# Kernel optimization log

Hardware: AMD Instinct MI355X
Metric: run time of the kernel (lower is better)

Reference implementation:

```python
import jax, jax.numpy as jnp
import numpy as np

N = 5000          # ngenes / nodes
IN_DIM = 1280
H = 128           # hid_dim
E = 160000        # edges (before self-loops)
ALPHA = 0.2       # LeakyReLU slope (both module leakyrelu and GATv2 negative_slope)

def _glorot(key, shape):
    fan_in, fan_out = shape[0], shape[-1]
    lim = jnp.sqrt(6.0 / (fan_in + fan_out))
    return jax.random.uniform(key, shape, jnp.float32, -lim, lim)

def setup_inputs() -> dict:
    key = jax.random.key(0)
    ks = jax.random.split(key, 12)
    x = jax.random.normal(ks[0], (N, IN_DIM), jnp.float32)
    edge_index = jax.random.randint(ks[1], (2, E), 0, N, jnp.int64)
    return {
        "x": x,
        "edge_index": edge_index,
        "W_in": _glorot(ks[2], (IN_DIM, H)),
        "b_in": jnp.zeros((H,), jnp.float32),
        "W_l": _glorot(ks[3], (H, H)),
        "b_l": jnp.zeros((H,), jnp.float32),
        "W_r": _glorot(ks[4], (H, H)),
        "b_r": jnp.zeros((H,), jnp.float32),
        "att": _glorot(ks[5], (H, 1))[:, 0],
        "gat_bias": jnp.zeros((H,), jnp.float32),
        "W1": _glorot(ks[6], (N * H, H)),
        "b1": jnp.zeros((H,), jnp.float32),
        "W2": _glorot(ks[7], (H, 1)),
        "b2": jnp.zeros((1,), jnp.float32),
    }

def _leaky(v):
    return jnp.where(v >= 0, v, ALPHA * v)

def _gatv2(x, edge_index, W_l, b_l, W_r, b_r, att, gat_bias):
    # add self loops (PyG default)
    loop = jnp.arange(N, dtype=edge_index.dtype)
    src = jnp.concatenate([edge_index[0], loop])  # j: source of message
    dst = jnp.concatenate([edge_index[1], loop])  # i: target / softmax segment
    xl = x @ W_l + b_l                             # [N, H] (messages)
    xr = x @ W_r + b_r                             # [N, H] (target side)
    e = _leaky(xl[src] + xr[dst])                  # [E+N, H]
    score = e @ att                                # [E+N]
    # segment softmax over incoming edges of each dst node
    m = jax.ops.segment_max(score, dst, num_segments=N)
    ex = jnp.exp(score - m[dst])
    s = jax.ops.segment_sum(ex, dst, num_segments=N)
    a = ex / s[dst]                                # [E+N]
    out = jax.ops.segment_sum(a[:, None] * xl[src], dst, num_segments=N)
    return out + gat_bias

def reference(x, edge_index, W_in, b_in, W_l, b_l, W_r, b_r, att, gat_bias, W1, b1, W2, b2):
    h = jax.nn.relu(x @ W_in + b_in)                               # [N, H]
    h = _leaky(_gatv2(h, edge_index, W_l, b_l, W_r, b_r, att, gat_bias))
    h = h.reshape(-1)                                              # [N*H]
    h = jax.nn.relu(h @ W1 + b1)                                   # [H]
    return h @ W2 + b2                                             # [1]
```

## Files before the change

### kernel.cpp

```cpp
#include <hip/hip_runtime.h>
#include <math.h>

#define N_NODES 5000
#define IN_DIM  1280
#define HID     128
#define ALPHA   0.2f

__device__ __forceinline__ float leaky(float v) { return v >= 0.f ? v : ALPHA * v; }

__global__ __launch_bounds__(256) void k_gemm_in(const float* __restrict__ x,
    const float* __restrict__ W, float* __restrict__ hp) {
  const int col  = threadIdx.x & 127;
  const int rg   = threadIdx.x >> 7;
  const int row0 = blockIdx.x * 16;
  const int kbase = blockIdx.y * 640;
  __shared__ float xs[16][128];
  float acc[8] = {0.f,0.f,0.f,0.f,0.f,0.f,0.f,0.f};
  for (int k0 = 0; k0 < 640; k0 += 128) {
#pragma unroll
    for (int t = 0; t < 8; ++t) {
      int idx = threadIdx.x + t * 256;
      int r = idx >> 7, c = idx & 127;
      int row = row0 + r;
      xs[r][c] = (row < N_NODES) ? x[(size_t)row * IN_DIM + kbase + k0 + c] : 0.f;
    }
    __syncthreads();
#pragma unroll 8
    for (int kq = 0; kq < 32; ++kq) {
      const int kk = kbase + k0 + kq * 4;
      const float w0 = W[(kk + 0) * HID + col];
      const float w1 = W[(kk + 1) * HID + col];
      const float w2 = W[(kk + 2) * HID + col];
      const float w3 = W[(kk + 3) * HID + col];
#pragma unroll
      for (int r = 0; r < 8; ++r) {
        const float4 xv = *reinterpret_cast<const float4*>(&xs[rg * 8 + r][kq * 4]);
        acc[r] = fmaf(xv.x, w0, acc[r]);
        acc[r] = fmaf(xv.y, w1, acc[r]);
        acc[r] = fmaf(xv.z, w2, acc[r]);
        acc[r] = fmaf(xv.w, w3, acc[r]);
      }
    }
    __syncthreads();
  }
  float* out = hp + (size_t)blockIdx.y * N_NODES * HID;
#pragma unroll
  for (int r = 0; r < 8; ++r) {
    int row = row0 + rg * 8 + r;
    if (row < N_NODES) out[(size_t)row * HID + col] = acc[r];
  }
}

__global__ __launch_bounds__(256) void k_gemm_lr(const float* __restrict__ hp,
    const float* __restrict__ bin,
    const float* __restrict__ Wl, const float* __restrict__ bl,
    const float* __restrict__ Wr, const float* __restrict__ br,
    float* __restrict__ xl, float* __restrict__ xr) {
  const int col  = threadIdx.x & 127;
  const int rg   = threadIdx.x >> 7;
  const int row0 = blockIdx.x * 8;
  __shared__ float hs[8][128];
  const float* hp0 = hp;
  const float* hp1 = hp + (size_t)N_NODES * HID;
#pragma unroll
  for (int t = 0; t < 4; ++t) {
    int idx = threadIdx.x + t * 256;
    int r = idx >> 7, c = idx & 127;
    size_t g = (size_t)(row0 + r) * HID + c;
    hs[r][c] = fmaxf(hp0[g] + hp1[g] + bin[c], 0.f);
  }
  __syncthreads();
  float accl[4] = {0.f,0.f,0.f,0.f};
  float accr[4] = {0.f,0.f,0.f,0.f};
#pragma unroll 4
  for (int kq = 0; kq < 32; ++kq) {
    float wl0 = Wl[(kq*4+0)*HID + col], wr0 = Wr[(kq*4+0)*HID + col];
    float wl1 = Wl[(kq*4+1)*HID + col], wr1 = Wr[(kq*4+1)*HID + col];
    float wl2 = Wl[(kq*4+2)*HID + col], wr2 = Wr[(kq*4+2)*HID + col];
    float wl3 = Wl[(kq*4+3)*HID + col], wr3 = Wr[(kq*4+3)*HID + col];
#pragma unroll
    for (int r = 0; r < 4; ++r) {
      const float4 xv = *reinterpret_cast<const float4*>(&hs[rg*4 + r][kq*4]);
      accl[r] = fmaf(xv.x, wl0, accl[r]); accr[r] = fmaf(xv.x, wr0, accr[r]);
      accl[r] = fmaf(xv.y, wl1, accl[r]); accr[r] = fmaf(xv.y, wr1, accr[r]);
      accl[r] = fmaf(xv.z, wl2, accl[r]); accr[r] = fmaf(xv.z, wr2, accr[r]);
      accl[r] = fmaf(xv.w, wl3, accl[r]); accr[r] = fmaf(xv.w, wr3, accr[r]);
    }
  }
  const float biasl = bl[col], biasr = br[col];
#pragma unroll
  for (int r = 0; r < 4; ++r) {
    int row = row0 + rg * 4 + r;
    xl[(size_t)row * HID + col] = accl[r] + biasl;
    xr[(size_t)row * HID + col] = accr[r] + biasr;
  }
}

__global__ __launch_bounds__(256) void k_hist(const int* __restrict__ ei, int E, int ET,
                                              unsigned* __restrict__ deg) {
  int e = blockIdx.x * blockDim.x + threadIdx.x;
  if (e >= ET) return;
  const int dst = (e < E) ? ei[E + e] : (e - E);
  atomicAdd(&deg[dst], 1u);
}

__global__ __launch_bounds__(256) void k_scan(const unsigned* __restrict__ deg,
    unsigned* __restrict__ off, unsigned* __restrict__ cursor) {
  __shared__ unsigned part[256];
  const int t = threadIdx.x;
  unsigned s = 0;
#pragma unroll
  for (int i = 0; i < 20; ++i) { int d = t * 20 + i; if (d < N_NODES) s += deg[d]; }
  part[t] = s;
  __syncthreads();
  for (int st = 1; st < 256; st <<= 1) {
    unsigned val = (t >= st) ? part[t - st] : 0u;
    __syncthreads();
    part[t] += val;
    __syncthreads();
  }
  unsigned run = (t == 0) ? 0u : part[t - 1];
  for (int i = 0; i < 20; ++i) {
    int d = t * 20 + i;
    if (d < N_NODES) { off[d] = run; cursor[d] = run; run += deg[d]; }
  }
}

__global__ __launch_bounds__(256) void k_fill(const int* __restrict__ ei, int E, int ET,
    unsigned* __restrict__ cursor, unsigned* __restrict__ csr) {
  int e = blockIdx.x * blockDim.x + threadIdx.x;
  if (e >= ET) return;
  const int src = (e < E) ? ei[e]     : (e - E);
  const int dst = (e < E) ? ei[E + e] : (e - E);
  unsigned pos = atomicAdd(&cursor[dst], 1u);
  csr[pos] = (unsigned)src;
}

__global__ __launch_bounds__(64) void k_agg(const float* __restrict__ xl,
    const float* __restrict__ xr, const float* __restrict__ att,
    const float* __restrict__ gb, const unsigned* __restrict__ off,
    const unsigned* __restrict__ deg, const unsigned* __restrict__ csr,
    float* __restrict__ v) {
  const int dst  = blockIdx.x;
  const int lane = threadIdx.x;
  const unsigned o  = off[dst];
  const unsigned dg = deg[dst];
  const float2 xr2 = *reinterpret_cast<const float2*>(&xr[(size_t)dst * HID + lane * 2]);
  const float2 at2 = *reinterpret_cast<const float2*>(&att[lane * 2]);
  float m = -INFINITY, s = 0.f;
  float2 acc = make_float2(0.f, 0.f);
  for (unsigned t = 0; t < dg; ++t) {
    const unsigned src = csr[o + t];
    const float2 xl2 = *reinterpret_cast<const float2*>(&xl[(size_t)src * HID + lane * 2]);
    float sa = leaky(xl2.x + xr2.x) * at2.x + leaky(xl2.y + xr2.y) * at2.y;
#pragma unroll
    for (int st = 1; st < 64; st <<= 1) sa += __shfl_xor(sa, st);
    if (sa > m) {
      const float sc = __expf(m - sa);
      s = s * sc + 1.f;
      acc.x = acc.x * sc + xl2.x;
      acc.y = acc.y * sc + xl2.y;
      m = sa;
    } else {
      const float ex = __expf(sa - m);
      s += ex;
      acc.x = fmaf(ex, xl2.x, acc.x);
      acc.y = fmaf(ex, xl2.y, acc.y);
    }
  }
  const float inv = 1.f / s;
  const float2 gb2 = *reinterpret_cast<const float2*>(&gb[lane * 2]);
  float2 r;
  r.x = leaky(fmaf(acc.x, inv, gb2.x));
  r.y = leaky(fmaf(acc.y, inv, gb2.y));
  *reinterpret_cast<float2*>(&v[(size_t)dst * HID + lane * 2]) = r;
}

__global__ __launch_bounds__(256) void k_matvec(const float* __restrict__ v,
    const float* __restrict__ W1, float* __restrict__ out128) {
  const int c  = threadIdx.x & 31;
  const int rr = threadIdx.x >> 5;
  const int base = blockIdx.x * 320;
  __shared__ float vs[320];
  if (threadIdx.x < 256) vs[threadIdx.x] = v[base + threadIdx.x];
  if (threadIdx.x < 64)  vs[256 + threadIdx.x] = v[base + 256 + threadIdx.x];
  __syncthreads();
  float4 acc = make_float4(0.f, 0.f, 0.f, 0.f);
#pragma unroll 8
  for (int it = 0; it < 40; ++it) {
    const int r = it * 8 + rr;
    const float4 w = *reinterpret_cast<const float4*>(&W1[(size_t)(base + r) * HID + c * 4]);
    const float vv = vs[r];
    acc.x = fmaf(vv, w.x, acc.x);
    acc.y = fmaf(vv, w.y, acc.y);
    acc.z = fmaf(vv, w.z, acc.z);
    acc.w = fmaf(vv, w.w, acc.w);
  }
  __shared__ float part[8][128];
  *reinterpret_cast<float4*>(&part[rr][c * 4]) = acc;
  __syncthreads();
  if (rr == 0) {
    float4 sum = make_float4(0.f, 0.f, 0.f, 0.f);
#pragma unroll
    for (int g = 0; g < 8; ++g) {
      const float4 p = *reinterpret_cast<const float4*>(&part[g][c * 4]);
      sum.x += p.x; sum.y += p.y; sum.z += p.z; sum.w += p.w;
    }
    atomicAdd(&out128[c * 4 + 0], sum.x);
    atomicAdd(&out128[c * 4 + 1], sum.y);
    atomicAdd(&out128[c * 4 + 2], sum.z);
    atomicAdd(&out128[c * 4 + 3], sum.w);
  }
}

__global__ void k_final(const float* __restrict__ out128, const float* __restrict__ b1,
                        const float* __restrict__ W2, const float* __restrict__ b2,
                        float* __restrict__ out) {
  __shared__ float red[128];
  const int j = threadIdx.x;
  const float y = fmaxf(out128[j] + b1[j], 0.f);
  red[j] = y * W2[j];
  __syncthreads();
  if (j == 0) {
    float t = 0.f;
    for (int k = 0; k < 128; ++k) t += red[k];
    out[0] = t + b2[0];
  }
}

extern "C" void kernel_launch(void* const* d_in, const int* in_sizes, int n_in,
                              void* d_out, int out_size, void* d_ws, size_t ws_size,
                              hipStream_t stream) {
  const float* x    = (const float*)d_in[0];
  const int*   ei   = (const int*)  d_in[1];
  const float* W_in = (const float*)d_in[2];
  const float* b_in = (const float*)d_in[3];
  const float* W_l  = (const float*)d_in[4];
  const float* b_l  = (const float*)d_in[5];
  const float* W_r  = (const float*)d_in[6];
  const float* b_r  = (const float*)d_in[7];
  const float* att  = (const float*)d_in[8];
  const float* gb   = (const float*)d_in[9];
  const float* W1   = (const float*)d_in[10];
  const float* b1   = (const float*)d_in[11];
  const float* W2   = (const float*)d_in[12];
  const float* b2   = (const float*)d_in[13];
  float* out = (float*)d_out;

  const int E  = in_sizes[1] / 2;
  const int ET = E + N_NODES;

  float* ws = (float*)d_ws;
  float*    hp     = ws;
  float*    xl     = ws + 1280000;
  float*    xr     = ws + 1920000;
  float*    v      = ws + 2560000;
  unsigned* deg    = (unsigned*)(ws + 3200000);
  unsigned* off    = deg + N_NODES;
  unsigned* cursor = off + N_NODES;
  unsigned* csr    = cursor + N_NODES;
  float*    out128 = (float*)(csr + ET);

  hipMemsetAsync(deg,    0, (size_t)N_NODES * sizeof(unsigned), stream);
  hipMemsetAsync(out128, 0, (size_t)HID * sizeof(float), stream);

  k_gemm_in <<<dim3((N_NODES + 15) / 16, 2), 256, 0, stream>>>(x, W_in, hp);
  k_gemm_lr <<<N_NODES / 8, 256, 0, stream>>>(hp, b_in, W_l, b_l, W_r, b_r, xl, xr);
  k_hist    <<<(ET + 255) / 256, 256, 0, stream>>>(ei, E, ET, deg);
  k_scan    <<<1, 256, 0, stream>>>(deg, off, cursor);
  k_fill    <<<(ET + 255) / 256, 256, 0, stream>>>(ei, E, ET, cursor, csr);
  k_agg     <<<N_NODES, 64, 0, stream>>>(xl, xr, att, gb, off, deg, csr, v);
  k_matvec  <<<2000, 256, 0, stream>>>(v, W1, out128);
  k_final   <<<1, 128, 0, stream>>>(out128, b1, W2, b2, out);
}
```

Baseline: 736.6 us.

## Prefetch W1 with nontemporal loads, shrink input GEMM tile, merge memsets

The W1 matvec now keeps eight float4 loads in flight through a rotating register buffer and uses nontemporal loads, so the 328 MB W1 stream is not limited by load latency and does not pollute cache. The input GEMM tile drops from 16 to 8 rows per block, doubling the block count for better occupancy at the cost of reading W_in more often. out128 is moved next to deg so a single memset clears both, and float4 is replaced by clang ext_vector_type. The bounds checks are removed because 5000 divides evenly by 8.

```diff
diff --git a/kernel.cpp b/kernel.cpp
--- a/kernel.cpp
+++ b/kernel.cpp
@@ -6,23 +6,24 @@
 #define HID     128
 #define ALPHA   0.2f
 
+typedef float f4v __attribute__((ext_vector_type(4)));
+
 __device__ __forceinline__ float leaky(float v) { return v >= 0.f ? v : ALPHA * v; }
 
 __global__ __launch_bounds__(256) void k_gemm_in(const float* __restrict__ x,
     const float* __restrict__ W, float* __restrict__ hp) {
   const int col  = threadIdx.x & 127;
   const int rg   = threadIdx.x >> 7;
-  const int row0 = blockIdx.x * 16;
+  const int row0 = blockIdx.x * 8;
   const int kbase = blockIdx.y * 640;
-  __shared__ float xs[16][128];
-  float acc[8] = {0.f,0.f,0.f,0.f,0.f,0.f,0.f,0.f};
+  __shared__ float xs[8][128];
+  float acc[4] = {0.f,0.f,0.f,0.f};
   for (int k0 = 0; k0 < 640; k0 += 128) {
 #pragma unroll
-    for (int t = 0; t < 8; ++t) {
+    for (int t = 0; t < 4; ++t) {
       int idx = threadIdx.x + t * 256;
-      int r = idx >> 7, c = idx & 127;
-      int row = row0 + r;
-      xs[r][c] = (row < N_NODES) ? x[(size_t)row * IN_DIM + kbase + k0 + c] : 0.f;
+      int r = idx >> 7, cc = idx & 127;
+      xs[r][cc] = x[(size_t)(row0 + r) * IN_DIM + kbase + k0 + cc];
     }
     __syncthreads();
 #pragma unroll 8
@@ -33,8 +34,8 @@
       const float w2 = W[(kk + 2) * HID + col];
       const float w3 = W[(kk + 3) * HID + col];
 #pragma unroll
-      for (int r = 0; r < 8; ++r) {
-        const float4 xv = *reinterpret_cast<const float4*>(&xs[rg * 8 + r][kq * 4]);
+      for (int r = 0; r < 4; ++r) {
+        const f4v xv = *reinterpret_cast<const f4v*>(&xs[rg * 4 + r][kq * 4]);
         acc[r] = fmaf(xv.x, w0, acc[r]);
         acc[r] = fmaf(xv.y, w1, acc[r]);
         acc[r] = fmaf(xv.z, w2, acc[r]);
@@ -43,12 +44,10 @@
     }
     __syncthreads();
   }
-  float* out = hp + (size_t)blockIdx.y * N_NODES * HID;
-#pragma unroll
-  for (int r = 0; r < 8; ++r) {
-    int row = row0 + rg * 8 + r;
-    if (row < N_NODES) out[(size_t)row * HID + col] = acc[r];
-  }
+  float* o = hp + (size_t)blockIdx.y * N_NODES * HID;
+#pragma unroll
+  for (int r = 0; r < 4; ++r)
+    o[(size_t)(row0 + rg * 4 + r) * HID + col] = acc[r];
 }
 
 __global__ __launch_bounds__(256) void k_gemm_lr(const float* __restrict__ hp,
@@ -80,7 +79,7 @@
     float wl3 = Wl[(kq*4+3)*HID + col], wr3 = Wr[(kq*4+3)*HID + col];
 #pragma unroll
     for (int r = 0; r < 4; ++r) {
-      const float4 xv = *reinterpret_cast<const float4*>(&hs[rg*4 + r][kq*4]);
+      const f4v xv = *reinterpret_cast<const f4v*>(&hs[rg*4 + r][kq*4]);
       accl[r] = fmaf(xv.x, wl0, accl[r]); accr[r] = fmaf(xv.x, wr0, accr[r]);
       accl[r] = fmaf(xv.y, wl1, accl[r]); accr[r] = fmaf(xv.y, wr1, accr[r]);
       accl[r] = fmaf(xv.z, wl2, accl[r]); accr[r] = fmaf(xv.z, wr2, accr[r]);
@@ -185,25 +184,32 @@
   if (threadIdx.x < 256) vs[threadIdx.x] = v[base + threadIdx.x];
   if (threadIdx.x < 64)  vs[256 + threadIdx.x] = v[base + 256 + threadIdx.x];
   __syncthreads();
-  float4 acc = make_float4(0.f, 0.f, 0.f, 0.f);
-#pragma unroll 8
-  for (int it = 0; it < 40; ++it) {
-    const int r = it * 8 + rr;
-    const float4 w = *reinterpret_cast<const float4*>(&W1[(size_t)(base + r) * HID + c * 4]);
-    const float vv = vs[r];
+  const float* Wp = W1 + (size_t)(base + rr) * HID + c * 4;
+  f4v pf[8];
+#pragma unroll
+  for (int p = 0; p < 8; ++p)
+    pf[p] = __builtin_nontemporal_load(reinterpret_cast<const f4v*>(Wp + (size_t)p * 8 * HID));
+  f4v acc = {0.f, 0.f, 0.f, 0.f};
+#pragma unroll
+  for (int i = 0; i < 40; ++i) {
+    const f4v w = pf[i & 7];
+    if (i + 8 < 40)
+      pf[i & 7] = __builtin_nontemporal_load(
+          reinterpret_cast<const f4v*>(Wp + (size_t)(i + 8) * 8 * HID));
+    const float vv = vs[i * 8 + rr];
     acc.x = fmaf(vv, w.x, acc.x);
     acc.y = fmaf(vv, w.y, acc.y);
     acc.z = fmaf(vv, w.z, acc.z);
     acc.w = fmaf(vv, w.w, acc.w);
   }
   __shared__ float part[8][128];
-  *reinterpret_cast<float4*>(&part[rr][c * 4]) = acc;
+  *reinterpret_cast<f4v*>(&part[rr][c * 4]) = acc;
   __syncthreads();
   if (rr == 0) {
-    float4 sum = make_float4(0.f, 0.f, 0.f, 0.f);
+    f4v sum = {0.f, 0.f, 0.f, 0.f};
 #pragma unroll
     for (int g = 0; g < 8; ++g) {
-      const float4 p = *reinterpret_cast<const float4*>(&part[g][c * 4]);
+      const f4v p = *reinterpret_cast<const f4v*>(&part[g][c * 4]);
       sum.x += p.x; sum.y += p.y; sum.z += p.z; sum.w += p.w;
     }
     atomicAdd(&out128[c * 4 + 0], sum.x);
@@ -256,15 +262,14 @@
   float*    xr     = ws + 1920000;
   float*    v      = ws + 2560000;
   unsigned* deg    = (unsigned*)(ws + 3200000);
-  unsigned* off    = deg + N_NODES;
+  float*    out128 = ws + 3200000 + N_NODES;
+  unsigned* off    = (unsigned*)(out128 + HID);
   unsigned* cursor = off + N_NODES;
   unsigned* csr    = cursor + N_NODES;
-  float*    out128 = (float*)(csr + ET);
-
-  hipMemsetAsync(deg,    0, (size_t)N_NODES * sizeof(unsigned), stream);
-  hipMemsetAsync(out128, 0, (size_t)HID * sizeof(float), stream);
-
-  k_gemm_in <<<dim3((N_NODES + 15) / 16, 2), 256, 0, stream>>>(x, W_in, hp);
+
+  hipMemsetAsync(deg, 0, (size_t)(N_NODES + HID) * sizeof(unsigned), stream);
+
+  k_gemm_in <<<dim3(N_NODES / 8, 2), 256, 0, stream>>>(x, W_in, hp);
   k_gemm_lr <<<N_NODES / 8, 256, 0, stream>>>(hp, b_in, W_l, b_l, W_r, b_r, xl, xr);
   k_hist    <<<(ET + 255) / 256, 256, 0, stream>>>(ei, E, ET, deg);
   k_scan    <<<1, 256, 0, stream>>>(deg, off, cursor);
```

Measured after the change: 763.0 us. 1.04x slower.
